# Kernel tuning notes

Measured on AMD Instinct MI355X. Metric: run time of the kernel, lower is better.

Reference implementation:

```python
import jax, jax.numpy as jnp
import numpy as np

K = 7          # kernel_size
PAD = K // 2   # padding


def _unfold(t):
    """im2col for kxk neighborhood: (B,C,H,W) -> (B,C,K*K,H,W), zero-padded."""
    B, C, H, W = t.shape
    p = jnp.pad(t, ((0, 0), (0, 0), (PAD, PAD), (PAD, PAD)))
    # row-major over kernel offsets matches F.unfold ordering
    wins = jnp.stack([p[:, :, i:i + H, j:j + W]
                      for i in range(K) for j in range(K)], axis=2)
    return wins


def setup_inputs() -> dict:
    key = jax.random.key(0)
    ks = jax.random.split(key, 7)
    B, C, H, W = 8, 128, 64, 64
    scale = 1.0 / np.sqrt(C)
    x = jax.random.normal(ks[0], (B, C, H, W), dtype=jnp.float32)
    Wq = jax.random.normal(ks[1], (C, C), dtype=jnp.float32) * scale
    Wk = jax.random.normal(ks[2], (C, C), dtype=jnp.float32) * scale
    Wv = jax.random.normal(ks[3], (C, C), dtype=jnp.float32) * scale
    bq = jax.random.normal(ks[4], (C,), dtype=jnp.float32) * 0.01
    bk = jax.random.normal(ks[5], (C,), dtype=jnp.float32) * 0.01
    bv = jax.random.normal(ks[6], (C,), dtype=jnp.float32) * 0.01
    return {"x": x, "Wq": Wq, "bq": bq, "Wk": Wk, "bk": bk, "Wv": Wv, "bv": bv}


def reference(x, Wq, bq, Wk, bk, Wv, bv):
    # 1x1 convs = channel GEMMs
    q = jnp.einsum('oc,bchw->bohw', Wq, x) + bq[:, None, None]
    k = jnp.einsum('oc,bchw->bohw', Wk, x) + bk[:, None, None]
    v = jnp.einsum('oc,bchw->bohw', Wv, x) + bv[:, None, None]
    k_unf = _unfold(k)   # (B,C,K*K,H,W)
    v_unf = _unfold(v)   # (B,C,K*K,H,W)
    # attention scores over the K*K neighborhood, summed over channels
    attn = jnp.einsum('bchw,bcphw->bphw', q, k_unf)
    attn = jax.nn.softmax(attn, axis=1)
    y = jnp.einsum('bphw,bcphw->bchw', attn, v_unf)
    return y
```

## Files before the change

kernel.cpp:

```cpp
#include <hip/hip_runtime.h>

#define CC   128
#define HH_  64
#define WW_  64
#define BB   8
#define HWSZ (HH_*WW_)
#define CHW  (CC*HWSZ)
#define BCHW (BB*CHW)
#define PAD  3
#define NP   49

__global__ __launch_bounds__(128) void qkv_proj(
    const float* __restrict__ x,
    const float* __restrict__ Wq, const float* __restrict__ bq,
    const float* __restrict__ Wk, const float* __restrict__ bk,
    const float* __restrict__ Wv, const float* __restrict__ bv,
    float* __restrict__ qkv)
{
    __shared__ float xs[32][132];
    __shared__ float ws[32][68];
    const int pt  = blockIdx.x;
    const int og  = blockIdx.y;
    const int b   = pt >> 5;
    const int hw0 = (pt & 31) << 7;
    const int tid = threadIdx.x;

    const int proj = og >> 1;
    const int row0 = (og & 1) << 6;
    const float* Wp = (proj == 0) ? Wq : (proj == 1 ? Wk : Wv);
    const float* Bp = (proj == 0) ? bq : (proj == 1 ? bk : bv);

    const int o8  = (tid >> 4) << 3;
    const int px4 = (tid & 15) << 2;

    float acc[8][8];
    #pragma unroll
    for (int j = 0; j < 8; ++j) {
        float bj = Bp[row0 + o8 + j];
        #pragma unroll
        for (int i = 0; i < 8; ++i) acc[j][i] = bj;
    }

    const float* xb = x + (size_t)b*CHW + hw0;

    for (int ck = 0; ck < 4; ++ck) {
        const int c0 = ck << 5;
        __syncthreads();
        #pragma unroll
        for (int i = 0; i < 8; ++i) {
            int f  = tid + (i << 7);
            int c  = f >> 5, q4 = (f & 31) << 2;
            *(float4*)&xs[c][q4] = *(const float4*)&xb[(size_t)(c0 + c)*HWSZ + q4];
        }
        #pragma unroll
        for (int i = 0; i < 4; ++i) {
            int f = tid + (i << 7);
            int o = f >> 3, c4 = (f & 7) << 2;
            float4 wv = *(const float4*)&Wp[(size_t)(row0 + o)*CC + c0 + c4];
            ws[c4+0][o] = wv.x; ws[c4+1][o] = wv.y;
            ws[c4+2][o] = wv.z; ws[c4+3][o] = wv.w;
        }
        __syncthreads();

        #pragma unroll 8
        for (int c = 0; c < 32; ++c) {
            float4 w0 = *(const float4*)&ws[c][o8];
            float4 w1 = *(const float4*)&ws[c][o8 + 4];
            float4 x0 = *(const float4*)&xs[c][px4];
            float4 x1 = *(const float4*)&xs[c][px4 + 64];
            float wr[8] = {w0.x,w0.y,w0.z,w0.w,w1.x,w1.y,w1.z,w1.w};
            float xr[8] = {x0.x,x0.y,x0.z,x0.w,x1.x,x1.y,x1.z,x1.w};
            #pragma unroll
            for (int j = 0; j < 8; ++j)
                #pragma unroll
                for (int i = 0; i < 8; ++i)
                    acc[j][i] = fmaf(wr[j], xr[i], acc[j][i]);
        }
    }

    float* op = qkv + (size_t)proj*BCHW + (size_t)b*CHW + hw0;
    #pragma unroll
    for (int j = 0; j < 8; ++j) {
        const int row = row0 + o8 + j;
        float4 s0 = make_float4(acc[j][0], acc[j][1], acc[j][2], acc[j][3]);
        float4 s1 = make_float4(acc[j][4], acc[j][5], acc[j][6], acc[j][7]);
        *(float4*)&op[(size_t)row*HWSZ + px4]      = s0;
        *(float4*)&op[(size_t)row*HWSZ + px4 + 64] = s1;
    }
}

__device__ __forceinline__ void load_chunk8(const float* __restrict__ src,
                                            int h0, int c0, float4* stg) {
    const int tid = threadIdx.x;
    #pragma unroll
    for (int i = 0; i < 4; ++i) {
        int f   = tid + (i << 9);
        int c   = f >> 7;
        int rem = f & 127;
        int r   = rem >> 4;
        int q4  = (rem & 15) << 2;
        int hh  = h0 - PAD + r;
        if ((unsigned)hh < (unsigned)HH_)
            stg[i] = *(const float4*)&src[(size_t)(c0 + c)*HWSZ + hh*WW_ + q4];
        else
            stg[i] = make_float4(0.f, 0.f, 0.f, 0.f);
    }
}

__device__ __forceinline__ void store_chunk8(float (*ks)[8][72], const float4* stg) {
    const int tid = threadIdx.x;
    #pragma unroll
    for (int i = 0; i < 4; ++i) {
        int f   = tid + (i << 9);
        int c   = f >> 7;
        int rem = f & 127;
        int r   = rem >> 4;
        int q4  = (rem & 15) << 2;
        *(float4*)&ks[c][r][4 + q4] = stg[i];
    }
}

__global__ __launch_bounds__(512) void locatt(
    const float* __restrict__ qkv, float* __restrict__ out)
{
    __shared__ float ks[16][8][72];
    __shared__ float lg[2][NP][64];
    __shared__ float dn[2][64];

    const int blk = blockIdx.x;
    const int x   = blk & 7;
    const int j   = blk >> 3;
    const int b   = j >> 2;
    const int h0  = (((x << 2) | (j & 3)) << 1);
    const int tid = threadIdx.x;
    const int s   = tid >> 6;
    const int w   = tid & 63;

    const float* qp = qkv + (size_t)b*CHW;
    const float* kp = qkv + (size_t)BCHW + (size_t)b*CHW;
    const float* vp = qkv + (size_t)2*BCHW + (size_t)b*CHW;

    if (tid < 256) {
        int idx = tid & 127;
        int c = idx >> 3, r = idx & 7;
        int col = (tid < 128) ? 0 : 68;
        *(float4*)&ks[c][r][col] = make_float4(0.f, 0.f, 0.f, 0.f);
    }

    const bool do0 = (s < 7);
    const bool do1 = (s >= 1);

    float acc0[7], acc1[7];
    #pragma unroll
    for (int dx = 0; dx < 7; ++dx) { acc0[dx] = 0.f; acc1[dx] = 0.f; }

    float4 stg[4];
    load_chunk8(kp, h0, 0, stg);

    for (int ck = 0; ck < 8; ++ck) {
        store_chunk8(ks, stg);
        __syncthreads();
        if (ck < 7) load_chunk8(kp, h0, (ck + 1) * 16, stg);

        const int c0 = ck << 4;
        float q0[16], q1[16];
        #pragma unroll
        for (int ci = 0; ci < 16; ++ci) {
            const float* qc = qp + (size_t)(c0 + ci)*HWSZ + h0*WW_ + w;
            q0[ci] = do0 ? qc[0]   : 0.f;
            q1[ci] = do1 ? qc[WW_] : 0.f;
        }

        const float* kbase = &ks[0][s][w + 1];
        #pragma unroll
        for (int ci = 0; ci < 16; ++ci) {
            const float* kc = kbase + ci * 576;
            #pragma unroll
            for (int dx = 0; dx < 7; ++dx) {
                float kv = kc[dx];
                acc0[dx] = fmaf(q0[ci], kv, acc0[dx]);
                acc1[dx] = fmaf(q1[ci], kv, acc1[dx]);
            }
        }
        __syncthreads();
    }

    #pragma unroll
    for (int dx = 0; dx < 7; ++dx) {
        if (do0) lg[0][s*7 + dx][w]       = acc0[dx];
        if (do1) lg[1][(s-1)*7 + dx][w]   = acc1[dx];
    }
    load_chunk8(vp, h0, 0, stg);
    __syncthreads();

    if (tid < 128) {
        const int r = tid >> 6, px = tid & 63;
        float tv[NP];
        float m = -1e30f;
        #pragma unroll
        for (int p = 0; p < NP; ++p) { tv[p] = lg[r][p][px]; m = fmaxf(m, tv[p]); }
        float d = 0.f;
        #pragma unroll
        for (int p = 0; p < NP; ++p) {
            float e = __expf(tv[p] - m);
            d += e;
            lg[r][p][px] = e;
        }
        dn[r][px] = 1.f / d;
    }
    __syncthreads();

    float a0[NP], a1[NP];
    const float sc0 = dn[0][w], sc1 = dn[1][w];
    #pragma unroll
    for (int p = 0; p < NP; ++p) a0[p] = lg[0][p][w] * sc0;
    #pragma unroll
    for (int p = 0; p < NP; ++p) a1[p] = lg[1][p][w] * sc1;

    for (int ck = 0; ck < 8; ++ck) {
        store_chunk8(ks, stg);
        __syncthreads();
        if (ck < 7) load_chunk8(vp, h0, (ck + 1) * 16, stg);

        #pragma unroll
        for (int half = 0; half < 2; ++half) {
            const int cl = s + (half << 3);
            float y0 = 0.f, y1 = 0.f;
            #pragma unroll
            for (int r = 0; r < 8; ++r) {
                const float* vr = &ks[cl][r][w + 1];
                #pragma unroll
                for (int dx = 0; dx < 7; ++dx) {
                    float vv = vr[dx];
                    if (r < 7)  y0 = fmaf(a0[r*7 + dx], vv, y0);
                    if (r >= 1) y1 = fmaf(a1[(r-1)*7 + dx], vv, y1);
                }
            }
            float* op = out + (size_t)b*CHW + (size_t)(ck*16 + cl)*HWSZ
                            + (size_t)h0*WW_ + w;
            op[0]   = y0;
            op[WW_] = y1;
        }
        __syncthreads();
    }
}

extern "C" void kernel_launch(void* const* d_in, const int* in_sizes, int n_in,
                              void* d_out, int out_size, void* d_ws, size_t ws_size,
                              hipStream_t stream) {
    const float* x  = (const float*)d_in[0];
    const float* Wq = (const float*)d_in[1];
    const float* bq = (const float*)d_in[2];
    const float* Wk = (const float*)d_in[3];
    const float* bk = (const float*)d_in[4];
    const float* Wv = (const float*)d_in[5];
    const float* bv = (const float*)d_in[6];
    float* out = (float*)d_out;
    float* qkv = (float*)d_ws;

    qkv_proj<<<dim3(256, 6), 128, 0, stream>>>(x, Wq, bq, Wk, bk, Wv, bv, qkv);
    locatt  <<<256, 512, 0, stream>>>(qkv, out);
}
```

Measured before the change: 150.8 us.

## Replace FP32 QKV projection with split-bf16 three-pass MFMA GEMM

Converts weights into high/low bf16 pairs in a small prep kernel and splits activations into hi/lo bf16 inside the GEMM kernel. The QKV projection then runs on MFMA 16x16x32 bf16 instructions in three passes (hi*hi, hi*lo, lo*hi) to approximate FP32 accuracy. The aim is to replace scalar FMA work with matrix-core throughput. The cost is an extra launch, staging the split weights in the output buffer as scratch, transposed LDS writes, and stores with uncoalesced per-row scalar writes.

```diff
diff --git a/kernel.cpp b/kernel.cpp
--- a/kernel.cpp
+++ b/kernel.cpp
@@ -1,4 +1,5 @@
 #include <hip/hip_runtime.h>
+#include <hip/hip_bf16.h>
 
 #define CC   128
 #define HH_  64
@@ -10,82 +11,120 @@
 #define PAD  3
 #define NP   49
 
-__global__ __launch_bounds__(128) void qkv_proj(
+typedef __attribute__((ext_vector_type(8))) short short8;
+typedef __attribute__((ext_vector_type(4))) float float4v;
+
+__global__ __launch_bounds__(256) void prep_w(
+    const float* __restrict__ Wq, const float* __restrict__ Wk,
+    const float* __restrict__ Wv,
+    unsigned short* __restrict__ whi, unsigned short* __restrict__ wlo)
+{
+    int i = blockIdx.x * 256 + threadIdx.x;
+    const float* src = (i < 16384) ? Wq : (i < 32768 ? Wk : Wv);
+    float f = src[i & 16383];
+    __hip_bfloat16 h = __float2bfloat16(f);
+    float hf = __bfloat162float(h);
+    __hip_bfloat16 l = __float2bfloat16(f - hf);
+    unsigned short hu, lu;
+    __builtin_memcpy(&hu, &h, 2);
+    __builtin_memcpy(&lu, &l, 2);
+    whi[i] = hu;
+    wlo[i] = lu;
+}
+
+__global__ __launch_bounds__(256, 2) void qkv_mfma(
     const float* __restrict__ x,
-    const float* __restrict__ Wq, const float* __restrict__ bq,
-    const float* __restrict__ Wk, const float* __restrict__ bk,
-    const float* __restrict__ Wv, const float* __restrict__ bv,
-    float* __restrict__ qkv)
+    const unsigned short* __restrict__ whi, const unsigned short* __restrict__ wlo,
+    const float* __restrict__ bq, const float* __restrict__ bk,
+    const float* __restrict__ bv, float* __restrict__ qkv)
 {
-    __shared__ float xs[32][132];
-    __shared__ float ws[32][68];
-    const int pt  = blockIdx.x;
-    const int og  = blockIdx.y;
-    const int b   = pt >> 5;
-    const int hw0 = (pt & 31) << 7;
-    const int tid = threadIdx.x;
-
-    const int proj = og >> 1;
-    const int row0 = (og & 1) << 6;
-    const float* Wp = (proj == 0) ? Wq : (proj == 1 ? Wk : Wv);
+    __shared__ unsigned short xT[2][128][136];
+    const int proj = blockIdx.y;
+    const int n0g  = blockIdx.x << 7;
+    const int b    = n0g >> 12;
+    const int npx  = n0g & 4095;
+    const int tid  = threadIdx.x;
+    const int lane = tid & 63;
+    const int wv   = tid >> 6;
+    const int wm   = wv & 1, wn = wv >> 1;
+
+    const float* xb = x + (size_t)b*CHW + npx;
+    #pragma unroll
+    for (int it = 0; it < 16; ++it) {
+        int f  = tid + (it << 8);
+        int c  = f >> 5;
+        int p4 = (f & 31) << 2;
+        float4 v = *(const float4*)&xb[(size_t)c*HWSZ + p4];
+        float vv[4] = {v.x, v.y, v.z, v.w};
+        #pragma unroll
+        for (int u = 0; u < 4; ++u) {
+            __hip_bfloat16 h = __float2bfloat16(vv[u]);
+            float hf = __bfloat162float(h);
+            __hip_bfloat16 l = __float2bfloat16(vv[u] - hf);
+            unsigned short hu, lu;
+            __builtin_memcpy(&hu, &h, 2);
+            __builtin_memcpy(&lu, &l, 2);
+            xT[0][p4 + u][c] = hu;
+            xT[1][p4 + u][c] = lu;
+        }
+    }
+
     const float* Bp = (proj == 0) ? bq : (proj == 1 ? bk : bv);
-
-    const int o8  = (tid >> 4) << 3;
-    const int px4 = (tid & 15) << 2;
-
-    float acc[8][8];
-    #pragma unroll
-    for (int j = 0; j < 8; ++j) {
-        float bj = Bp[row0 + o8 + j];
-        #pragma unroll
-        for (int i = 0; i < 8; ++i) acc[j][i] = bj;
-    }
-
-    const float* xb = x + (size_t)b*CHW + hw0;
-
-    for (int ck = 0; ck < 4; ++ck) {
-        const int c0 = ck << 5;
-        __syncthreads();
-        #pragma unroll
-        for (int i = 0; i < 8; ++i) {
-            int f  = tid + (i << 7);
-            int c  = f >> 5, q4 = (f & 31) << 2;
-            *(float4*)&xs[c][q4] = *(const float4*)&xb[(size_t)(c0 + c)*HWSZ + q4];
-        }
-        #pragma unroll
-        for (int i = 0; i < 4; ++i) {
-            int f = tid + (i << 7);
-            int o = f >> 3, c4 = (f & 7) << 2;
-            float4 wv = *(const float4*)&Wp[(size_t)(row0 + o)*CC + c0 + c4];
-            ws[c4+0][o] = wv.x; ws[c4+1][o] = wv.y;
-            ws[c4+2][o] = wv.z; ws[c4+3][o] = wv.w;
-        }
-        __syncthreads();
-
-        #pragma unroll 8
-        for (int c = 0; c < 32; ++c) {
-            float4 w0 = *(const float4*)&ws[c][o8];
-            float4 w1 = *(const float4*)&ws[c][o8 + 4];
-            float4 x0 = *(const float4*)&xs[c][px4];
-            float4 x1 = *(const float4*)&xs[c][px4 + 64];
-            float wr[8] = {w0.x,w0.y,w0.z,w0.w,w1.x,w1.y,w1.z,w1.w};
-            float xr[8] = {x0.x,x0.y,x0.z,x0.w,x1.x,x1.y,x1.z,x1.w};
-            #pragma unroll
-            for (int j = 0; j < 8; ++j)
+    const int q4 = lane >> 4;
+    float4v acc[4][4];
+    #pragma unroll
+    for (int sm = 0; sm < 4; ++sm) {
+        const int mb = wm*64 + sm*16 + q4*4;
+        float4v bi;
+        bi[0] = Bp[mb+0]; bi[1] = Bp[mb+1]; bi[2] = Bp[mb+2]; bi[3] = Bp[mb+3];
+        #pragma unroll
+        for (int sn = 0; sn < 4; ++sn) acc[sm][sn] = bi;
+    }
+
+    __syncthreads();
+
+    const unsigned short* Wh = whi + (size_t)proj*16384;
+    const unsigned short* Wl = wlo + (size_t)proj*16384;
+    const int kq8  = q4 << 3;
+    const int mrow = lane & 15;
+
+    for (int pass = 0; pass < 3; ++pass) {
+        const unsigned short* Wp = (pass == 2) ? Wl : Wh;
+        const int xi = (pass == 1) ? 1 : 0;
+        #pragma unroll
+        for (int kc = 0; kc < 4; ++kc) {
+            const int kb = kc << 5;
+            short8 a[4], bf[4];
+            #pragma unroll
+            for (int sm = 0; sm < 4; ++sm) {
+                const int m = wm*64 + sm*16 + mrow;
+                a[sm] = *(const short8*)&Wp[(size_t)m*CC + kb + kq8];
+            }
+            #pragma unroll
+            for (int sn = 0; sn < 4; ++sn) {
+                const int n = wn*64 + sn*16 + mrow;
+                bf[sn] = *(const short8*)&xT[xi][n][kb + kq8];
+            }
+            #pragma unroll
+            for (int sm = 0; sm < 4; ++sm)
                 #pragma unroll
-                for (int i = 0; i < 8; ++i)
-                    acc[j][i] = fmaf(wr[j], xr[i], acc[j][i]);
-        }
-    }
-
-    float* op = qkv + (size_t)proj*BCHW + (size_t)b*CHW + hw0;
-    #pragma unroll
-    for (int j = 0; j < 8; ++j) {
-        const int row = row0 + o8 + j;
-        float4 s0 = make_float4(acc[j][0], acc[j][1], acc[j][2], acc[j][3]);
-        float4 s1 = make_float4(acc[j][4], acc[j][5], acc[j][6], acc[j][7]);
-        *(float4*)&op[(size_t)row*HWSZ + px4]      = s0;
-        *(float4*)&op[(size_t)row*HWSZ + px4 + 64] = s1;
+                for (int sn = 0; sn < 4; ++sn)
+                    acc[sm][sn] = __builtin_amdgcn_mfma_f32_16x16x32_bf16(
+                        a[sm], bf[sn], acc[sm][sn], 0, 0, 0);
+        }
+    }
+
+    float* op = qkv + (size_t)proj*BCHW + (size_t)b*CHW + npx;
+    #pragma unroll
+    for (int sm = 0; sm < 4; ++sm) {
+        const int mb = wm*64 + sm*16 + q4*4;
+        #pragma unroll
+        for (int sn = 0; sn < 4; ++sn) {
+            const int n = wn*64 + sn*16 + mrow;
+            #pragma unroll
+            for (int r = 0; r < 4; ++r)
+                op[(size_t)(mb + r)*HWSZ + n] = acc[sm][sn][r];
+        }
     }
 }
 
@@ -187,8 +226,8 @@
 
     #pragma unroll
     for (int dx = 0; dx < 7; ++dx) {
-        if (do0) lg[0][s*7 + dx][w]       = acc0[dx];
-        if (do1) lg[1][(s-1)*7 + dx][w]   = acc1[dx];
+        if (do0) lg[0][s*7 + dx][w]     = acc0[dx];
+        if (do1) lg[1][(s-1)*7 + dx][w] = acc1[dx];
     }
     load_chunk8(vp, h0, 0, stg);
     __syncthreads();
@@ -258,6 +297,10 @@
     float* out = (float*)d_out;
     float* qkv = (float*)d_ws;
 
-    qkv_proj<<<dim3(256, 6), 128, 0, stream>>>(x, Wq, bq, Wk, bk, Wv, bv, qkv);
+    unsigned short* whi = (unsigned short*)d_out;
+    unsigned short* wlo = whi + 3*16384;
+
+    prep_w  <<<192, 256, 0, stream>>>(Wq, Wk, Wv, whi, wlo);
+    qkv_mfma<<<dim3(256, 3), 256, 0, stream>>>(x, whi, wlo, bq, bk, bv, qkv);
     locatt  <<<256, 512, 0, stream>>>(qkv, out);
 }
```

New measurement: 144.6 us. 1.04x faster.
